# Kernel tuning notes

Hardware: AMD Instinct MI355X
Metric: run time of the kernel (lower is better)

The kernel has to match this reference:

```python
import jax, jax.numpy as jnp
import numpy as np

B, T, D = 4, 2048, 1024
NF = 512
NB = 4
FREQ_SCALE = 0.1


def _w(k, shape, scale):
    return jax.random.normal(k, shape, jnp.float32) * scale


def setup_inputs() -> dict:
    key = jax.random.key(0)
    ks = jax.random.split(key, 16)
    d = D ** -0.5
    inp = {}
    inp['x'] = jax.random.normal(ks[0], (B, T, D), jnp.float32)
    inp['norm_g'] = jnp.ones((D,), jnp.float32)
    inp['norm_b'] = jnp.zeros((D,), jnp.float32)
    inp['Wconcept'] = _w(ks[1], (D, D), d); inp['bconcept'] = jnp.zeros((D,), jnp.float32)
    inp['Wcg'] = _w(ks[2], (D, D), d); inp['bcg'] = jnp.zeros((D,), jnp.float32)
    inp['Wfg'] = _w(ks[3], (NF, D), d); inp['bfg'] = jnp.zeros((NF,), jnp.float32)
    inp['Wtg'] = _w(ks[4], (1, D), d); inp['btg'] = jnp.zeros((1,), jnp.float32)
    inp['Wband'] = _w(ks[5], (NB, D), d); inp['bband'] = jnp.zeros((NB,), jnp.float32)
    inp['Wsp'] = _w(ks[6], (2 * NF, D), d)  # to_spectral, no bias
    inp['freq_importance'] = jnp.ones((NF,), jnp.float32)
    inp['log_decay'] = (jnp.linspace(-3.0, -0.001, NF) + _w(ks[7], (NF,), 0.1)).astype(jnp.float32)
    inp['frequencies'] = ((jnp.arange(NF, dtype=jnp.float32) / NF * 2.0 - 1.0) * 0.2)
    inp['dt'] = jnp.ones((NF,), jnp.float32) * 0.5
    inp['Wgate'] = _w(ks[8], (D, D), d); inp['bgate'] = jnp.zeros((D,), jnp.float32)
    inp['Wfs'] = _w(ks[9], (D, 2 * NF), (2 * NF) ** -0.5)  # from_spectral, no bias
    inp['output_scale'] = jnp.ones((1,), jnp.float32) * 0.5
    inp['norm2_g'] = jnp.ones((D,), jnp.float32)
    inp['norm2_b'] = jnp.zeros((D,), jnp.float32)
    inp['W1'] = _w(ks[10], (4 * D, D), d); inp['b1'] = jnp.zeros((4 * D,), jnp.float32)
    inp['W2'] = _w(ks[11], (D, 4 * D), (4 * D) ** -0.5); inp['b2'] = jnp.zeros((D,), jnp.float32)
    return inp


def _ln(x, g, b):
    m = jnp.mean(x, axis=-1, keepdims=True)
    v = jnp.var(x, axis=-1, keepdims=True)
    return (x - m) * jax.lax.rsqrt(v + 1e-5) * g + b


def reference(x, norm_g, norm_b, Wconcept, bconcept, Wcg, bcg, Wfg, bfg, Wtg, btg,
              Wband, bband, Wsp, freq_importance, log_decay, frequencies, dt,
              Wgate, bgate, Wfs, output_scale, norm2_g, norm2_b, W1, b1, W2, b2):
    b_, t_, _ = x.shape
    nf = log_decay.shape[0]
    nb = Wband.shape[0]
    residual = x
    xn = _ln(x, norm_g, norm_b)

    concept = xn @ Wconcept.T + bconcept
    concept_preserved = concept * jax.nn.sigmoid(xn @ Wcg.T + bcg)

    forget_gates = jax.nn.sigmoid(xn @ Wfg.T + bfg)          # (B,T,NF)
    temporal_strength = jax.nn.sigmoid(xn @ Wtg.T + btg)     # (B,T,1)
    band_strengths = jax.nn.sigmoid(xn @ Wband.T + bband)    # (B,T,NB)

    sp = xn @ Wsp.T                                          # (B,T,2*NF)
    u = jax.lax.complex(sp[..., :nf], sp[..., nf:]) * forget_gates

    decay = jax.nn.sigmoid(log_decay) * (jax.nn.softmax(freq_importance) * nf)
    omega = frequencies * FREQ_SCALE * (jax.nn.sigmoid(dt) * 2.0)
    rot = jax.lax.complex(jnp.cos(omega), jnp.sin(omega))    # (NF,)
    A = decay * rot                                          # (NF,) complex

    band_scale = jnp.repeat(band_strengths, nf // nb, axis=-1)  # (B,T,NF)
    A_exp = A * band_scale                                   # (B,T,NF) complex

    ones_first = jnp.ones((b_, 1, nf), A_exp.dtype)
    powers = jnp.cumprod(jnp.concatenate([ones_first, A_exp[:, :-1, :]], axis=1), axis=1)
    powers = powers * temporal_strength
    kernel = powers * rot

    n_fft = 2 * t_
    Uf = jnp.fft.fft(u, n=n_fft, axis=1)
    Kf = jnp.fft.fft(kernel, n=n_fft, axis=1)
    y = jnp.fft.ifft(Uf * Kf, n=n_fft, axis=1)[:, :t_, :]

    spectral_out = jnp.concatenate([y.real, y.imag], axis=-1)
    y_proj = (spectral_out @ Wfs.T) * output_scale
    gate_values = jax.nn.sigmoid(xn @ Wgate.T + bgate)
    y_gated = (y_proj * gate_values + concept_preserved) / 2.0  # dropout: eval mode

    x2 = residual + y_gated
    xn2 = _ln(x2, norm2_g, norm2_b)
    h = jax.nn.gelu(xn2 @ W1.T + b1, approximate=False)
    return x2 + h @ W2.T + b2
```

## Files before the change

kernel.cpp:

```cpp
#include <hip/hip_runtime.h>
#include <hip/hip_bf16.h>
#include <cstdint>
#include <cstddef>

typedef unsigned short u16;
typedef unsigned int u32;
typedef short bf16x8 __attribute__((ext_vector_type(8)));
typedef float f32x4 __attribute__((ext_vector_type(4)));
typedef float f32x2 __attribute__((ext_vector_type(2)));

static constexpr int Bb = 4, Tt = 2048, Dd = 1024, NFf = 512, NBb = 4;
static constexpr int Mm = Bb * Tt;
static constexpr int NZz = 4736;
static constexpr int Lc = 32;

#define DEV __device__ __forceinline__

typedef const __attribute__((address_space(1))) u32* gas_p;
typedef __attribute__((address_space(3))) u32* las_p;

DEV u16 f2bf(float f) {
    uint32_t u = __float_as_uint(f);
    u = (u + 0x7FFF + ((u >> 16) & 1)) >> 16;
    return (u16)u;
}
DEV float bf2f(u16 h) { return __uint_as_float(((uint32_t)h) << 16); }
DEV float sigm(float x) { return 1.0f / (1.0f + __expf(-x)); }
DEV float gelu_ex(float t) { return 0.5f * t * (1.0f + erff(t * 0.70710678118f)); }

static constexpr int NW0 = NZz * Dd;
static constexpr int NW1 = Dd * 2 * NFf;
static constexpr int NW2 = 4 * Dd * Dd;
static constexpr int NW3 = 4 * Dd * Dd;
static constexpr int NWTOT = NW0 + NW1 + NW2 + NW3;
static constexpr int NWB = NWTOT / 256;

__global__ __launch_bounds__(256) void prep_all(
    const float* __restrict__ Wconcept, const float* __restrict__ Wcg,
    const float* __restrict__ Wfg, const float* __restrict__ Wgate,
    const float* __restrict__ Wsp, const float* __restrict__ Wtg,
    const float* __restrict__ Wband,
    const float* __restrict__ bconcept, const float* __restrict__ bcg,
    const float* __restrict__ bfg, const float* __restrict__ bgate,
    const float* __restrict__ btg, const float* __restrict__ bband,
    const float* __restrict__ Wfs, const float* __restrict__ W1,
    const float* __restrict__ W2,
    const float* __restrict__ fi, const float* __restrict__ logd,
    const float* __restrict__ freqs, const float* __restrict__ dtv,
    const float* __restrict__ x, const float* __restrict__ norm_g,
    const float* __restrict__ norm_b,
    u16* __restrict__ wcat, float* __restrict__ bias_cat,
    u16* __restrict__ wfs, u16* __restrict__ w1b, u16* __restrict__ w2b,
    float* __restrict__ rr, float* __restrict__ ri,
    float* __restrict__ Ar, float* __restrict__ Ai,
    u16* __restrict__ xn)
{
    const int bx = blockIdx.x;
    if (bx == 0) {
        __shared__ float red[256];
        int t = threadIdx.x;
        float v0 = fi[t], v1 = fi[t + 256];
        red[t] = fmaxf(v0, v1); __syncthreads();
        for (int s = 128; s; s >>= 1) { if (t < s) red[t] = fmaxf(red[t], red[t + s]); __syncthreads(); }
        float mx = red[0]; __syncthreads();
        float e0 = expf(v0 - mx), e1 = expf(v1 - mx);
        red[t] = e0 + e1; __syncthreads();
        for (int s = 128; s; s >>= 1) { if (t < s) red[t] += red[t + s]; __syncthreads(); }
        float inv = 1.0f / red[0];
#pragma unroll
        for (int k = 0; k < 2; k++) {
            int f = t + k * 256;
            float e = k ? e1 : e0;
            float decay = sigm(logd[f]) * (e * inv * (float)NFf);
            float omega = freqs[f] * 0.1f * (sigm(dtv[f]) * 2.0f);
            float cc = cosf(omega), ss = sinf(omega);
            rr[f] = cc; ri[f] = ss; Ar[f] = decay * cc; Ai[f] = decay * ss;
        }
        return;
    }
    if (bx <= NWB) {
        int i = (bx - 1) * 256 + threadIdx.x;
        if (i < NW0) {
            int r = i >> 10, c = i & 1023;
            float v;
            if      (r < 1024) v = Wconcept[r * 1024 + c];
            else if (r < 2048) v = Wcg[(r - 1024) * 1024 + c];
            else if (r < 2560) v = Wfg[(r - 2048) * 1024 + c];
            else if (r < 3584) v = Wgate[(r - 2560) * 1024 + c];
            else if (r < 4608) v = Wsp[(r - 3584) * 1024 + c];
            else if (r == 4608) v = Wtg[c];
            else if (r < 4613) v = Wband[(r - 4609) * 1024 + c];
            else v = 0.0f;
            wcat[i] = f2bf(v);
            if (c == 0) {
                float bv;
                if      (r < 1024) bv = bconcept[r];
                else if (r < 2048) bv = bcg[r - 1024];
                else if (r < 2560) bv = bfg[r - 2048];
                else if (r < 3584) bv = bgate[r - 2560];
                else if (r < 4608) bv = 0.0f;
                else if (r == 4608) bv = btg[0];
                else if (r < 4613) bv = bband[r - 4609];
                else bv = 0.0f;
                bias_cat[r] = bv;
            }
        } else if (i < NW0 + NW1) {
            int j = i - NW0; wfs[j] = f2bf(Wfs[j]);
        } else if (i < NW0 + NW1 + NW2) {
            int j = i - NW0 - NW1; w1b[j] = f2bf(W1[j]);
        } else {
            int j = i - NW0 - NW1 - NW2; w2b[j] = f2bf(W2[j]);
        }
        return;
    }
    const int m = bx - NWB - 1, tid = threadIdx.x;
    float4 v = ((const float4*)(x + (size_t)m * Dd))[tid];
    float s1 = v.x + v.y + v.z + v.w;
    float s2 = v.x * v.x + v.y * v.y + v.z * v.z + v.w * v.w;
    __shared__ float lds[16];
    for (int o = 32; o; o >>= 1) { s1 += __shfl_down(s1, o); s2 += __shfl_down(s2, o); }
    int lane = tid & 63, w = tid >> 6;
    if (!lane) { lds[w] = s1; lds[8 + w] = s2; }
    __syncthreads();
    s1 = lds[0] + lds[1] + lds[2] + lds[3];
    s2 = lds[8] + lds[9] + lds[10] + lds[11];
    float mean = s1 * (1.0f / Dd);
    float var  = s2 * (1.0f / Dd) - mean * mean;
    float rstd = rsqrtf(var + 1e-5f);
    float4 gv = ((const float4*)norm_g)[tid];
    float4 bv = ((const float4*)norm_b)[tid];
    ushort4 o;
    o.x = f2bf((v.x - mean) * rstd * gv.x + bv.x);
    o.y = f2bf((v.y - mean) * rstd * gv.y + bv.y);
    o.z = f2bf((v.z - mean) * rstd * gv.z + bv.z);
    o.w = f2bf((v.w - mean) * rstd * gv.w + bv.w);
    ((ushort4*)(xn + (size_t)m * Dd))[tid] = o;
}

template<int MODE>
__global__ __launch_bounds__(256, 3) void gemm_bt(
    const u16* __restrict__ A, const u16* __restrict__ Bw,
    const float* __restrict__ bias, const u16* __restrict__ addb,
    void* __restrict__ Cout, int M, int N, int K)
{
    __shared__ __align__(16) u16 smA[128 * 64];
    __shared__ __align__(16) u16 smB[128 * 64];
    const int tid = threadIdx.x;
    const int m0 = blockIdx.x * 128;
    const int n0 = blockIdx.y * 128;
    const int w = tid >> 6, lane = tid & 63;
    const int wr = w >> 1, wc = w & 1;
    const int quad = lane >> 4, l16 = lane & 15;

    const int r0 = tid >> 3;
    const int cs = (tid & 7) ^ (r0 & 7);
    const u16* gA = A + (size_t)(m0 + r0) * K + cs * 8;
    const u16* gB = Bw + (size_t)(n0 + r0) * K + cs * 8;

    const int swzf = l16 & 7;

    f32x4 acc[4][4];
#pragma unroll
    for (int i = 0; i < 4; i++)
#pragma unroll
        for (int j = 0; j < 4; j++) acc[i][j] = {0.f, 0.f, 0.f, 0.f};

    for (int k0 = 0; k0 < K; k0 += 64) {
        __syncthreads();
#pragma unroll
        for (int j = 0; j < 4; j++) {
            __builtin_amdgcn_global_load_lds((gas_p)(gA + k0 + (size_t)(j * 32) * K),
                                             (las_p)(smA + j * 2048 + tid * 8), 16, 0, 0);
            __builtin_amdgcn_global_load_lds((gas_p)(gB + k0 + (size_t)(j * 32) * K),
                                             (las_p)(smB + j * 2048 + tid * 8), 16, 0, 0);
        }
        __syncthreads();
#pragma unroll
        for (int seg = 0; seg < 2; seg++) {
            bf16x8 af[4], bfv[4];
#pragma unroll
            for (int mi = 0; mi < 4; mi++)
                af[mi] = *(const bf16x8*)&smA[(wr * 64 + mi * 16 + l16) * 64 +
                                              (((seg * 4 + quad) ^ swzf) * 8)];
#pragma unroll
            for (int ni = 0; ni < 4; ni++)
                bfv[ni] = *(const bf16x8*)&smB[(wc * 64 + ni * 16 + l16) * 64 +
                                               (((seg * 4 + quad) ^ swzf) * 8)];
#pragma unroll
            for (int mi = 0; mi < 4; mi++)
#pragma unroll
                for (int ni = 0; ni < 4; ni++)
                    acc[mi][ni] = __builtin_amdgcn_mfma_f32_16x16x32_bf16(
                        af[mi], bfv[ni], acc[mi][ni], 0, 0, 0);
        }
    }

#pragma unroll
    for (int mi = 0; mi < 4; mi++) {
#pragma unroll
        for (int ni = 0; ni < 4; ni++) {
            const int gn = n0 + wc * 64 + ni * 16 + l16;
            const int gm0 = m0 + wr * 64 + mi * 16 + quad * 4;
            if constexpr (MODE == 0 || MODE == 2 || MODE == 4) {
                float bv = (MODE == 4) ? 0.0f : bias[gn];
                float t0 = acc[mi][ni][0] + bv, t1 = acc[mi][ni][1] + bv;
                float t2 = acc[mi][ni][2] + bv, t3 = acc[mi][ni][3] + bv;
                if constexpr (MODE == 2) {
                    t0 = gelu_ex(t0); t1 = gelu_ex(t1); t2 = gelu_ex(t2); t3 = gelu_ex(t3);
                }
                __hip_bfloat162 h01 = __float22bfloat162_rn(float2{t0, t1});
                __hip_bfloat162 h23 = __float22bfloat162_rn(float2{t2, t3});
                __hip_bfloat16* o = (__hip_bfloat16*)Cout;
                o[(size_t)(gm0 + 0) * N + gn] = h01.x;
                o[(size_t)(gm0 + 1) * N + gn] = h01.y;
                o[(size_t)(gm0 + 2) * N + gn] = h23.x;
                o[(size_t)(gm0 + 3) * N + gn] = h23.y;
            } else {
#pragma unroll
                for (int r = 0; r < 4; r++) {
                    const int gm = gm0 + r;
                    ((float*)Cout)[(size_t)gm * N + gn] =
                        acc[mi][ni][r] + bias[gn] + bf2f(addb[(size_t)gm * N + gn]);
                }
            }
        }
    }
}

static constexpr int NBLK_A = (Mm * NFf) / 256;

__global__ __launch_bounds__(256) void prepAk_kernel(
    const u16* __restrict__ Z, ushort2* __restrict__ u2b,
    const float* __restrict__ Ar, const float* __restrict__ Ai,
    const float* __restrict__ rr, const float* __restrict__ ri,
    f32x2* __restrict__ k2)
{
    const int bx = blockIdx.x;
    if (bx < NBLK_A) {
        int i = bx * 256 + threadIdx.x;
        int m = i >> 9, f = i & (NFf - 1);
        const u16* zr = Z + (size_t)m * NZz;
        float fg  = sigm(bf2f(zr[2048 + f]));
        float spr = bf2f(zr[3584 + f]);
        float spi = bf2f(zr[3584 + NFf + f]);
        u2b[i] = ushort2{f2bf(spr * fg), f2bf(spi * fg)};
        return;
    }
    int g = (bx - NBLK_A) * 256 + threadIdx.x;
    int b = g >> 9, f = g & (NFf - 1);
    float Pr = 1.0f, Pi = 0.0f;
    float ar = Ar[f], ai = Ai[f], cr = rr[f], ci = ri[f];
    const int band = f >> 7;
    const u16* zb = Z + (size_t)(b * Tt) * NZz;
    for (int tau = 0; tau < Lc; tau++) {
        const u16* zrow = zb + (size_t)tau * NZz;
        float tsv = sigm(bf2f(zrow[4608]));
        k2[((size_t)b * Lc + tau) * NFf + f] = f32x2{tsv * (cr * Pr - ci * Pi),
                                                     tsv * (cr * Pi + ci * Pr)};
        float bsv = sigm(bf2f(zrow[4609 + band]));
        float er = ar * bsv, ei = ai * bsv;
        float nPr = Pr * er - Pi * ei;
        float nPi = Pr * ei + Pi * er;
        Pr = nPr; Pi = nPi;
    }
}

__global__ __launch_bounds__(256) void conv_kernel(
    const ushort2* __restrict__ u2b, const f32x2* __restrict__ k2,
    u16* __restrict__ spec)
{
    __shared__ f32x2 su[96 * 64];
    __shared__ f32x2 sk[Lc * 64];
    const int tid = threadIdx.x;
    const int fl = tid & 63;
    const int ty = tid >> 6;
    const int f0 = blockIdx.x * 64;
    const int t0 = blockIdx.y * 64;
    const int b  = blockIdx.z;

    for (int i = tid; i < Lc * 64; i += 256) {
        int tau = i >> 6, ff = i & 63;
        sk[i] = k2[((size_t)b * Lc + tau) * NFf + f0 + ff];
    }
    for (int i = tid; i < 96 * 64; i += 256) {
        int r = i >> 6, ff = i & 63;
        int t = t0 - 32 + r;
        f32x2 v = {0.f, 0.f};
        if (t >= 0) {
            ushort2 h = u2b[((size_t)b * Tt + t) * NFf + f0 + ff];
            v = f32x2{bf2f(h.x), bf2f(h.y)};
        }
        su[i] = v;
    }
    __syncthreads();

    const int tl0 = 32 + ty * 16;
    f32x2 win[16], y[16];
#pragma unroll
    for (int j = 0; j < 16; j++) {
        win[j] = su[(tl0 + j) * 64 + fl];
        y[j] = f32x2{0.f, 0.f};
    }
#pragma unroll
    for (int tau = 0; tau < Lc; tau++) {
        f32x2 k = sk[tau * 64 + fl];
#pragma unroll
        for (int j = 0; j < 16; j++) {
            y[j].x += win[j].x * k.x - win[j].y * k.y;
            y[j].y += win[j].x * k.y + win[j].y * k.x;
        }
#pragma unroll
        for (int j = 15; j >= 1; j--) win[j] = win[j - 1];
        win[0] = su[(tl0 - tau - 1) * 64 + fl];
    }
#pragma unroll
    for (int j = 0; j < 16; j++) {
        size_t row = (size_t)(b * Tt + t0 + ty * 16 + j);
        spec[row * (2 * NFf) + f0 + fl]       = f2bf(y[j].x);
        spec[row * (2 * NFf) + NFf + f0 + fl] = f2bf(y[j].y);
    }
}

__global__ __launch_bounds__(256) void fuse2_ln_kernel(
    const float* __restrict__ x, const u16* __restrict__ Z,
    const u16* __restrict__ P2, const float* __restrict__ osc,
    const float* __restrict__ g2, const float* __restrict__ b2v,
    u16* __restrict__ x2b, u16* __restrict__ xn2)
{
    const int m = blockIdx.x, tid = threadIdx.x;
    const float os = osc[0];
    const u16* zr = Z + (size_t)m * NZz;
    float4 xv = ((const float4*)(x + (size_t)m * Dd))[tid];
    ushort4 pv = ((const ushort4*)(P2 + (size_t)m * Dd))[tid];
    float vals[4]; float s1 = 0.0f, s2 = 0.0f;
#pragma unroll
    for (int j = 0; j < 4; j++) {
        int d = tid * 4 + j;
        float concept = bf2f(zr[d]);
        float cg   = sigm(bf2f(zr[1024 + d]));
        float gate = sigm(bf2f(zr[2560 + d]));
        float p = bf2f((&pv.x)[j]);
        float v = (&xv.x)[j] + 0.5f * (p * os * gate + concept * cg);
        vals[j] = v; s1 += v; s2 += v * v;
    }
    __shared__ float lds[16];
    for (int o = 32; o; o >>= 1) { s1 += __shfl_down(s1, o); s2 += __shfl_down(s2, o); }
    int lane = tid & 63, w = tid >> 6;
    if (!lane) { lds[w] = s1; lds[8 + w] = s2; }
    __syncthreads();
    s1 = lds[0] + lds[1] + lds[2] + lds[3];
    s2 = lds[8] + lds[9] + lds[10] + lds[11];
    float mean = s1 * (1.0f / Dd);
    float var  = s2 * (1.0f / Dd) - mean * mean;
    float rstd = rsqrtf(var + 1e-5f);
    ushort4 xo, no;
#pragma unroll
    for (int j = 0; j < 4; j++) {
        int d = tid * 4 + j;
        (&xo.x)[j] = f2bf(vals[j]);
        (&no.x)[j] = f2bf((vals[j] - mean) * rstd * g2[d] + b2v[d]);
    }
    ((ushort4*)(x2b + (size_t)m * Dd))[tid] = xo;
    ((ushort4*)(xn2 + (size_t)m * Dd))[tid] = no;
}

extern "C" void kernel_launch(void* const* d_in, const int* in_sizes, int n_in,
                              void* d_out, int out_size, void* d_ws, size_t ws_size,
                              hipStream_t stream)
{
    const float* x        = (const float*)d_in[0];
    const float* norm_g   = (const float*)d_in[1];
    const float* norm_b   = (const float*)d_in[2];
    const float* Wconcept = (const float*)d_in[3];
    const float* bconcept = (const float*)d_in[4];
    const float* Wcg      = (const float*)d_in[5];
    const float* bcg      = (const float*)d_in[6];
    const float* Wfg      = (const float*)d_in[7];
    const float* bfg      = (const float*)d_in[8];
    const float* Wtg      = (const float*)d_in[9];
    const float* btg      = (const float*)d_in[10];
    const float* Wband    = (const float*)d_in[11];
    const float* bband    = (const float*)d_in[12];
    const float* Wsp      = (const float*)d_in[13];
    const float* fi       = (const float*)d_in[14];
    const float* logd     = (const float*)d_in[15];
    const float* freqs    = (const float*)d_in[16];
    const float* dtv      = (const float*)d_in[17];
    const float* Wgate    = (const float*)d_in[18];
    const float* bgate    = (const float*)d_in[19];
    const float* Wfs      = (const float*)d_in[20];
    const float* osc      = (const float*)d_in[21];
    const float* n2g      = (const float*)d_in[22];
    const float* n2b      = (const float*)d_in[23];
    const float* W1       = (const float*)d_in[24];
    const float* b1       = (const float*)d_in[25];
    const float* W2       = (const float*)d_in[26];
    const float* b2       = (const float*)d_in[27];

    char* ws = (char*)d_ws;
    size_t off = 0;
    auto alloc = [&](size_t bytes) { size_t c = off; off += (bytes + 255) & ~(size_t)255; return c; };
    size_t o_wcat = alloc((size_t)NZz * Dd * 2);
    size_t o_bias = alloc((size_t)NZz * 4);
    size_t o_wfs  = alloc((size_t)Dd * 2 * NFf * 2);
    size_t o_w1   = alloc((size_t)4 * Dd * Dd * 2);
    size_t o_w2   = alloc((size_t)4 * Dd * Dd * 2);
    size_t o_xn   = alloc((size_t)Mm * Dd * 2);
    size_t o_Z    = alloc((size_t)Mm * NZz * 2);
    size_t o_u    = alloc((size_t)Mm * NFf * 4);
    size_t o_spec = alloc((size_t)Mm * Dd * 2);
    size_t o_P2   = alloc((size_t)Mm * Dd * 2);
    size_t o_k2   = alloc((size_t)Bb * Lc * NFf * 8);
    size_t o_rr   = alloc(NFf * 4);
    size_t o_ri   = alloc(NFf * 4);
    size_t o_Ar   = alloc(NFf * 4);
    size_t o_Ai   = alloc(NFf * 4);
    if (ws_size < off) return;

    u16*    wcat = (u16*)(ws + o_wcat);
    float*  bias = (float*)(ws + o_bias);
    u16*    wfs  = (u16*)(ws + o_wfs);
    u16*    w1b  = (u16*)(ws + o_w1);
    u16*    w2b  = (u16*)(ws + o_w2);
    u16*    xn   = (u16*)(ws + o_xn);
    u16*    Zb   = (u16*)(ws + o_Z);
    u16*    hb   = (u16*)(ws + o_Z);
    ushort2* u2b = (ushort2*)(ws + o_u);
    u16*    x2b  = (u16*)(ws + o_u);
    u16*    spec = (u16*)(ws + o_spec);
    u16*    xn2  = (u16*)(ws + o_spec);
    u16*    P2   = (u16*)(ws + o_P2);
    f32x2*  k2   = (f32x2*)(ws + o_k2);
    float*  rr   = (float*)(ws + o_rr);
    float*  ri   = (float*)(ws + o_ri);
    float*  Ar   = (float*)(ws + o_Ar);
    float*  Ai   = (float*)(ws + o_Ai);

    prep_all<<<1 + NWB + Mm, 256, 0, stream>>>(
        Wconcept, Wcg, Wfg, Wgate, Wsp, Wtg, Wband,
        bconcept, bcg, bfg, bgate, btg, bband,
        Wfs, W1, W2, fi, logd, freqs, dtv,
        x, norm_g, norm_b,
        wcat, bias, wfs, w1b, w2b, rr, ri, Ar, Ai, xn);

    gemm_bt<0><<<dim3(Mm / 128, NZz / 128), 256, 0, stream>>>(
        xn, wcat, bias, nullptr, (void*)Zb, Mm, NZz, Dd);

    prepAk_kernel<<<NBLK_A + (Bb * NFf) / 256, 256, 0, stream>>>(
        Zb, u2b, Ar, Ai, rr, ri, k2);

    conv_kernel<<<dim3(NFf / 64, Tt / 64, Bb), 256, 0, stream>>>(u2b, k2, spec);

    gemm_bt<4><<<dim3(Mm / 128, Dd / 128), 256, 0, stream>>>(
        spec, wfs, nullptr, nullptr, (void*)P2, Mm, Dd, 2 * NFf);

    fuse2_ln_kernel<<<Mm, 256, 0, stream>>>(x, Zb, P2, osc, n2g, n2b, x2b, xn2);

    gemm_bt<2><<<dim3(Mm / 128, (4 * Dd) / 128), 256, 0, stream>>>(
        xn2, w1b, b1, nullptr, (void*)hb, Mm, 4 * Dd, Dd);
    gemm_bt<3><<<dim3(Mm / 128, Dd / 128), 256, 0, stream>>>(
        hb, w2b, b2, x2b, d_out, Mm, Dd, 4 * Dd);
}
```

Baseline: 528.2 us.

## Vectorize weight conversion and elementwise loads, add XCD-aware GEMM block swizzle

The weight-to-bf16 conversion in prep_all now handles four elements per thread with float4 loads and ushort4 stores, and launches a quarter as many blocks. prepAk and the fused LayerNorm kernel read bf16 gate and activation columns as packed vectors instead of scalar loads. The GEMM kernel remaps block indices so consecutive tiles land on the same XCD, aiming at better L2 reuse across the MI355X chiplets. Together these cut memory instruction count and scattered access, at the cost of assuming aligned, evenly divisible sizes.

```diff
diff --git a/kernel.cpp b/kernel.cpp
--- a/kernel.cpp
+++ b/kernel.cpp
@@ -28,12 +28,21 @@
 DEV float sigm(float x) { return 1.0f / (1.0f + __expf(-x)); }
 DEV float gelu_ex(float t) { return 0.5f * t * (1.0f + erff(t * 0.70710678118f)); }
 
+DEV void xcd_swizzle(int& bx, int& by) {
+    int gx = gridDim.x, nwg = gx * gridDim.y;
+    int lin = blockIdx.x + gx * blockIdx.y;
+    int q = nwg >> 3, r = nwg & 7;
+    int xcd = lin & 7, idx = lin >> 3;
+    int wg = (xcd < r) ? (xcd * (q + 1) + idx) : (r * (q + 1) + (xcd - r) * q + idx);
+    bx = wg % gx; by = wg / gx;
+}
+
 static constexpr int NW0 = NZz * Dd;
 static constexpr int NW1 = Dd * 2 * NFf;
 static constexpr int NW2 = 4 * Dd * Dd;
 static constexpr int NW3 = 4 * Dd * Dd;
 static constexpr int NWTOT = NW0 + NW1 + NW2 + NW3;
-static constexpr int NWB = NWTOT / 256;
+static constexpr int NWB4 = NWTOT / 1024;
 
 __global__ __launch_bounds__(256) void prep_all(
     const float* __restrict__ Wconcept, const float* __restrict__ Wcg,
@@ -78,20 +87,20 @@
         }
         return;
     }
-    if (bx <= NWB) {
-        int i = (bx - 1) * 256 + threadIdx.x;
+    if (bx <= NWB4) {
+        const int i = ((bx - 1) * 256 + threadIdx.x) * 4;
         if (i < NW0) {
             int r = i >> 10, c = i & 1023;
-            float v;
-            if      (r < 1024) v = Wconcept[r * 1024 + c];
-            else if (r < 2048) v = Wcg[(r - 1024) * 1024 + c];
-            else if (r < 2560) v = Wfg[(r - 2048) * 1024 + c];
-            else if (r < 3584) v = Wgate[(r - 2560) * 1024 + c];
-            else if (r < 4608) v = Wsp[(r - 3584) * 1024 + c];
-            else if (r == 4608) v = Wtg[c];
-            else if (r < 4613) v = Wband[(r - 4609) * 1024 + c];
-            else v = 0.0f;
-            wcat[i] = f2bf(v);
+            float4 v = {0.f, 0.f, 0.f, 0.f};
+            if      (r < 1024) v = *(const float4*)(Wconcept + r * 1024 + c);
+            else if (r < 2048) v = *(const float4*)(Wcg + (r - 1024) * 1024 + c);
+            else if (r < 2560) v = *(const float4*)(Wfg + (r - 2048) * 1024 + c);
+            else if (r < 3584) v = *(const float4*)(Wgate + (r - 2560) * 1024 + c);
+            else if (r < 4608) v = *(const float4*)(Wsp + (r - 3584) * 1024 + c);
+            else if (r == 4608) v = *(const float4*)(Wtg + c);
+            else if (r < 4613) v = *(const float4*)(Wband + (r - 4609) * 1024 + c);
+            ushort4 o{f2bf(v.x), f2bf(v.y), f2bf(v.z), f2bf(v.w)};
+            *(ushort4*)(wcat + i) = o;
             if (c == 0) {
                 float bv;
                 if      (r < 1024) bv = bconcept[r];
@@ -105,15 +114,21 @@
                 bias_cat[r] = bv;
             }
         } else if (i < NW0 + NW1) {
-            int j = i - NW0; wfs[j] = f2bf(Wfs[j]);
+            int j = i - NW0;
+            float4 v = *(const float4*)(Wfs + j);
+            *(ushort4*)(wfs + j) = ushort4{f2bf(v.x), f2bf(v.y), f2bf(v.z), f2bf(v.w)};
         } else if (i < NW0 + NW1 + NW2) {
-            int j = i - NW0 - NW1; w1b[j] = f2bf(W1[j]);
+            int j = i - NW0 - NW1;
+            float4 v = *(const float4*)(W1 + j);
+            *(ushort4*)(w1b + j) = ushort4{f2bf(v.x), f2bf(v.y), f2bf(v.z), f2bf(v.w)};
         } else {
-            int j = i - NW0 - NW1 - NW2; w2b[j] = f2bf(W2[j]);
+            int j = i - NW0 - NW1 - NW2;
+            float4 v = *(const float4*)(W2 + j);
+            *(ushort4*)(w2b + j) = ushort4{f2bf(v.x), f2bf(v.y), f2bf(v.z), f2bf(v.w)};
         }
         return;
     }
-    const int m = bx - NWB - 1, tid = threadIdx.x;
+    const int m = bx - NWB4 - 1, tid = threadIdx.x;
     float4 v = ((const float4*)(x + (size_t)m * Dd))[tid];
     float s1 = v.x + v.y + v.z + v.w;
     float s2 = v.x * v.x + v.y * v.y + v.z * v.z + v.w * v.w;
@@ -146,8 +161,10 @@
     __shared__ __align__(16) u16 smA[128 * 64];
     __shared__ __align__(16) u16 smB[128 * 64];
     const int tid = threadIdx.x;
-    const int m0 = blockIdx.x * 128;
-    const int n0 = blockIdx.y * 128;
+    int bxs, bys;
+    xcd_swizzle(bxs, bys);
+    const int m0 = bxs * 128;
+    const int n0 = bys * 128;
     const int w = tid >> 6, lane = tid & 63;
     const int wr = w >> 1, wc = w & 1;
     const int quad = lane >> 4, l16 = lane & 15;
@@ -227,8 +244,6 @@
     }
 }
 
-static constexpr int NBLK_A = (Mm * NFf) / 256;
-
 __global__ __launch_bounds__(256) void prepAk_kernel(
     const u16* __restrict__ Z, ushort2* __restrict__ u2b,
     const float* __restrict__ Ar, const float* __restrict__ Ai,
@@ -236,17 +251,20 @@
     f32x2* __restrict__ k2)
 {
     const int bx = blockIdx.x;
-    if (bx < NBLK_A) {
-        int i = bx * 256 + threadIdx.x;
-        int m = i >> 9, f = i & (NFf - 1);
+    if (bx < Mm) {
+        const int m = bx, t = threadIdx.x;
         const u16* zr = Z + (size_t)m * NZz;
-        float fg  = sigm(bf2f(zr[2048 + f]));
-        float spr = bf2f(zr[3584 + f]);
-        float spi = bf2f(zr[3584 + NFf + f]);
-        u2b[i] = ushort2{f2bf(spr * fg), f2bf(spi * fg)};
+        ushort2 fgh = *(const ushort2*)(zr + 2048 + 2 * t);
+        ushort2 spr = *(const ushort2*)(zr + 3584 + 2 * t);
+        ushort2 spi = *(const ushort2*)(zr + 4096 + 2 * t);
+        float fg0 = sigm(bf2f(fgh.x)), fg1 = sigm(bf2f(fgh.y));
+        ushort4 o;
+        o.x = f2bf(bf2f(spr.x) * fg0); o.y = f2bf(bf2f(spi.x) * fg0);
+        o.z = f2bf(bf2f(spr.y) * fg1); o.w = f2bf(bf2f(spi.y) * fg1);
+        ((ushort4*)u2b)[m * 256 + t] = o;
         return;
     }
-    int g = (bx - NBLK_A) * 256 + threadIdx.x;
+    int g = (bx - Mm) * 256 + threadIdx.x;
     int b = g >> 9, f = g & (NFf - 1);
     float Pr = 1.0f, Pi = 0.0f;
     float ar = Ar[f], ai = Ai[f], cr = rr[f], ci = ri[f];
@@ -332,13 +350,15 @@
     const u16* zr = Z + (size_t)m * NZz;
     float4 xv = ((const float4*)(x + (size_t)m * Dd))[tid];
     ushort4 pv = ((const ushort4*)(P2 + (size_t)m * Dd))[tid];
+    ushort4 cv = *(const ushort4*)(zr + tid * 4);
+    ushort4 gv = *(const ushort4*)(zr + 1024 + tid * 4);
+    ushort4 av = *(const ushort4*)(zr + 2560 + tid * 4);
     float vals[4]; float s1 = 0.0f, s2 = 0.0f;
 #pragma unroll
     for (int j = 0; j < 4; j++) {
-        int d = tid * 4 + j;
-        float concept = bf2f(zr[d]);
-        float cg   = sigm(bf2f(zr[1024 + d]));
-        float gate = sigm(bf2f(zr[2560 + d]));
+        float concept = bf2f((&cv.x)[j]);
+        float cg   = sigm(bf2f((&gv.x)[j]));
+        float gate = sigm(bf2f((&av.x)[j]));
         float p = bf2f((&pv.x)[j]);
         float v = (&xv.x)[j] + 0.5f * (p * os * gate + concept * cg);
         vals[j] = v; s1 += v; s2 += v * v;
@@ -436,7 +456,7 @@
     float*  Ar   = (float*)(ws + o_Ar);
     float*  Ai   = (float*)(ws + o_Ai);
 
-    prep_all<<<1 + NWB + Mm, 256, 0, stream>>>(
+    prep_all<<<1 + NWB4 + Mm, 256, 0, stream>>>(
         Wconcept, Wcg, Wfg, Wgate, Wsp, Wtg, Wband,
         bconcept, bcg, bfg, bgate, btg, bband,
         Wfs, W1, W2, fi, logd, freqs, dtv,
@@ -446,7 +466,7 @@
     gemm_bt<0><<<dim3(Mm / 128, NZz / 128), 256, 0, stream>>>(
         xn, wcat, bias, nullptr, (void*)Zb, Mm, NZz, Dd);
 
-    prepAk_kernel<<<NBLK_A + (Bb * NFf) / 256, 256, 0, stream>>>(
+    prepAk_kernel<<<Mm + (Bb * NFf) / 256, 256, 0, stream>>>(
         Zb, u2b, Ar, Ai, rr, ri, k2);
 
     conv_kernel<<<dim3(NFf / 64, Tt / 64, Bb), 256, 0, stream>>>(u2b, k2, spec);
```

Result: slower. 584.1 us (+10.6%).
